# Optimization experiments

Hardware: AMD Instinct MI355X
Metric: run time of the kernel (lower is better)

## Reference

```python
import jax, jax.numpy as jnp
import numpy as np

EPS = 1e-6
NUM_HEADS = 16

def rmsnorm(x, w):
    # x: [..., d], w: [d]
    norm = jax.lax.rsqrt(jnp.mean(x * x, axis=-1, keepdims=True) + EPS)
    return w * (x * norm)

def setup_inputs() -> dict:
    key = jax.random.key(0)
    ks = jax.random.split(key, 6)
    B, N, C = 2, 2048, 1024
    H = NUM_HEADS
    hd = C // H
    x = jax.random.normal(ks[0], (B, N, C), dtype=jnp.float32)
    scale = 1.0 / np.sqrt(C)
    qkv_w = jax.random.normal(ks[1], (C, 3 * C), dtype=jnp.float32) * scale
    qkv_b = jnp.zeros((3 * C,), dtype=jnp.float32)
    q_norm_w = jnp.ones((hd,), dtype=jnp.float32)
    k_norm_w = jnp.ones((hd,), dtype=jnp.float32)
    proj_w = jax.random.normal(ks[2], (C, C), dtype=jnp.float32) * scale
    proj_b = jnp.zeros((C,), dtype=jnp.float32)
    return {"x": x, "qkv_w": qkv_w, "qkv_b": qkv_b,
            "q_norm_w": q_norm_w, "k_norm_w": k_norm_w,
            "proj_w": proj_w, "proj_b": proj_b}

def reference(x, qkv_w, qkv_b, q_norm_w, k_norm_w, proj_w, proj_b):
    B, N, C = x.shape
    H = NUM_HEADS
    hd = C // H
    qkv = x @ qkv_w + qkv_b                       # [B,N,3C]
    qkv = qkv.reshape(B, N, 3, H, hd)
    q, k, v = qkv[:, :, 0], qkv[:, :, 1], qkv[:, :, 2]  # [B,N,H,hd]
    q = jnp.transpose(q, (0, 2, 1, 3))            # [B,H,N,hd]
    k = jnp.transpose(k, (0, 2, 1, 3))
    v = jnp.transpose(v, (0, 2, 1, 3))
    q = rmsnorm(q, q_norm_w)
    k = rmsnorm(k, k_norm_w)
    scores = jnp.einsum('bhqd,bhkd->bhqk', q, k) / jnp.sqrt(jnp.float32(hd))
    attn = jax.nn.softmax(scores, axis=-1)
    out = jnp.einsum('bhqk,bhkd->bhqd', attn, v)  # [B,H,N,hd]
    out = jnp.transpose(out, (0, 2, 1, 3)).reshape(B, N, C)
    return out @ proj_w + proj_b
```

## Files before the change

kernel.cpp:

```cpp
#include <hip/hip_runtime.h>

typedef unsigned short u16;
typedef unsigned int u32;
typedef __bf16 bf16x8 __attribute__((ext_vector_type(8)));
typedef float f32x4 __attribute__((ext_vector_type(4)));
typedef unsigned short u16x8 __attribute__((ext_vector_type(8)));
typedef unsigned short u16x4 __attribute__((ext_vector_type(4)));
typedef float f4 __attribute__((ext_vector_type(4)));

__device__ __forceinline__ float bf2f(u16 u) {
    union { unsigned int i; float f; } c; c.i = ((unsigned int)u) << 16; return c.f;
}
__device__ __forceinline__ u16 f2bf(float f) {
    union { float f; unsigned int i; } c; c.f = f;
    unsigned int r = c.i + 0x7FFFu + ((c.i >> 16) & 1u);
    return (u16)(r >> 16);
}
__device__ __forceinline__ u16 f2bf_rtz(float f) {
    union { float f; unsigned int i; } c; c.f = f;
    return (u16)(c.i >> 16);
}
__device__ __forceinline__ float fast_exp2(float x) {
#if __has_builtin(__builtin_amdgcn_exp2f)
    return __builtin_amdgcn_exp2f(x);
#else
    return exp2f(x);
#endif
}
__device__ __forceinline__ void async16(const void* g, void* l) {
    __builtin_amdgcn_global_load_lds(
        (const __attribute__((address_space(1))) u32*)g,
        (__attribute__((address_space(3))) u32*)l, 16, 0, 0);
}

__global__ __launch_bounds__(256) void cast_bf16(
    const float* __restrict__ X, u16* __restrict__ H)
{
    const size_t i = ((size_t)blockIdx.x * 256 + threadIdx.x) * 8;
    u16x8 h;
    #pragma unroll
    for (int e = 0; e < 8; ++e) h[e] = f2bf(X[i + e]);
    *(u16x8*)&H[i] = h;
}

__global__ __launch_bounds__(256) void transpose_cast(
    const float* __restrict__ W, u16* __restrict__ Th, int K, int N)
{
    __shared__ float tile[32][33];
    const int bk = blockIdx.y * 32, bn = blockIdx.x * 32;
    const int tx = threadIdx.x & 31, ty = threadIdx.x >> 5;
    #pragma unroll
    for (int r = ty; r < 32; r += 8)
        tile[r][tx] = W[(size_t)(bk + r) * N + bn + tx];
    __syncthreads();
    #pragma unroll
    for (int r = ty; r < 32; r += 8)
        Th[(size_t)(bn + r) * K + bk + tx] = f2bf(tile[tx][r]);
}

__global__ __launch_bounds__(256) void gemm_qkv(
    const u16* __restrict__ AH, const u16* __restrict__ BH,
    const float* __restrict__ bias,
    u16* __restrict__ Qb, u16* __restrict__ Kb, u16* __restrict__ Vt,
    const float* __restrict__ qw, const float* __restrict__ kw)
{
    const int K = 1024;
    __shared__ __align__(16) u16 AhT[128 * 32];
    __shared__ __align__(16) u16 BhT[128 * 32];
    const int t = threadIdx.x;
    const int bm = blockIdx.y * 128, bn = blockIdx.x * 128;
    const int wave = t >> 6, lane = t & 63;
    const int wm = (wave >> 1) * 64, wn = (wave & 1) * 64;
    const int l15 = lane & 15, quad = lane >> 4;
    const int srow = lane >> 2, scol = (lane & 3) * 8;

    f32x4 acc[4][4];
    const f32x4 zero = {0.0f, 0.0f, 0.0f, 0.0f};
    #pragma unroll
    for (int i = 0; i < 4; ++i)
        #pragma unroll
        for (int j = 0; j < 4; ++j) acc[i][j] = zero;

    for (int k0 = 0; k0 < K; k0 += 32) {
        #pragma unroll
        for (int rr = 0; rr < 2; ++rr) {
            const int r0 = (rr * 4 + wave) * 16;
            const size_t ga = (size_t)(bm + r0 + srow) * K + k0 + scol;
            const size_t gb = (size_t)(bn + r0 + srow) * K + k0 + scol;
            async16(&AH[ga], &AhT[r0 * 32]);
            async16(&BH[gb], &BhT[r0 * 32]);
        }
        __syncthreads();
        bf16x8 ah[4], bh[4];
        #pragma unroll
        for (int i = 0; i < 4; ++i)
            ah[i] = *(const bf16x8*)&AhT[(wm + i * 16 + l15) * 32 + quad * 8];
        #pragma unroll
        for (int j = 0; j < 4; ++j)
            bh[j] = *(const bf16x8*)&BhT[(wn + j * 16 + l15) * 32 + quad * 8];
        #pragma unroll
        for (int i = 0; i < 4; ++i)
            #pragma unroll
            for (int j = 0; j < 4; ++j)
                acc[i][j] = __builtin_amdgcn_mfma_f32_16x16x32_bf16(
                    ah[i], bh[j], acc[i][j], 0, 0, 0);
        __syncthreads();
    }

    const int gc0 = bn + wn;
    const int sec = gc0 >> 10;
    const int h = (gc0 & 1023) >> 6;
    const int b = bm >> 11;
    const int bhd = b * 16 + h;
    float bv[4], wj[4];
    #pragma unroll
    for (int j = 0; j < 4; ++j) {
        const int d = j * 16 + l15;
        bv[j] = bias[gc0 + d];
        wj[j] = (sec == 2) ? 0.0f : (sec ? kw[d] : qw[d] * 0.18033688011f);
    }
    if (sec < 2) {
        u16* dst = sec ? Kb : Qb;
        #pragma unroll
        for (int i = 0; i < 4; ++i) {
            float val[4][4];
            float ss[4] = {0.0f, 0.0f, 0.0f, 0.0f};
            #pragma unroll
            for (int j = 0; j < 4; ++j)
                #pragma unroll
                for (int r = 0; r < 4; ++r) {
                    val[j][r] = acc[i][j][r] + bv[j];
                    ss[r] += val[j][r] * val[j][r];
                }
            #pragma unroll
            for (int r = 0; r < 4; ++r) {
                #pragma unroll
                for (int m = 1; m < 16; m <<= 1)
                    ss[r] += __shfl_xor(ss[r], m, 64);
                const float nrm = rsqrtf(ss[r] * 0.015625f + 1e-6f);
                const int n = (bm + wm + i * 16 + quad * 4 + r) & 2047;
                const size_t rowb = ((size_t)bhd * 2048 + n) * 64;
                #pragma unroll
                for (int j = 0; j < 4; ++j)
                    dst[rowb + j * 16 + l15] = f2bf(val[j][r] * nrm * wj[j]);
            }
        }
    } else {
        #pragma unroll
        for (int i = 0; i < 4; ++i) {
            const int n0 = (bm + wm + i * 16 + quad * 4) & 2047;
            #pragma unroll
            for (int j = 0; j < 4; ++j) {
                const int d = j * 16 + l15;
                u16x4 pk;
                #pragma unroll
                for (int r = 0; r < 4; ++r)
                    pk[r] = f2bf(acc[i][j][r] + bv[j]);
                *(u16x4*)&Vt[((size_t)bhd * 64 + d) * 2048 + n0] = pk;
            }
        }
    }
}

__global__ __launch_bounds__(256) void gemm_proj(
    const u16* __restrict__ AH, const u16* __restrict__ BH,
    const float* __restrict__ bias, float* __restrict__ C)
{
    const int N = 1024, K = 1024;
    __shared__ __align__(16) u16 AhT[64 * 32];
    __shared__ __align__(16) u16 BhT[128 * 32];
    const int t = threadIdx.x;
    const int bm = blockIdx.y * 64, bn = blockIdx.x * 128;
    const int wave = t >> 6, lane = t & 63;
    const int l15 = lane & 15, quad = lane >> 4;
    const int srow = lane >> 2, scol = (lane & 3) * 8;

    f32x4 acc[4][2];
    const f32x4 zero = {0.0f, 0.0f, 0.0f, 0.0f};
    #pragma unroll
    for (int i = 0; i < 4; ++i)
        #pragma unroll
        for (int j = 0; j < 2; ++j) acc[i][j] = zero;

    for (int k0 = 0; k0 < K; k0 += 32) {
        {
            const int r0 = wave * 16;
            async16(&AH[(size_t)(bm + r0 + srow) * K + k0 + scol],
                    &AhT[r0 * 32]);
        }
        #pragma unroll
        for (int cc = 0; cc < 2; ++cc) {
            const int r0 = (wave * 2 + cc) * 16;
            async16(&BH[(size_t)(bn + r0 + srow) * K + k0 + scol],
                    &BhT[r0 * 32]);
        }
        __syncthreads();
        bf16x8 ah[4], bh[2];
        #pragma unroll
        for (int i = 0; i < 4; ++i)
            ah[i] = *(const bf16x8*)&AhT[(i * 16 + l15) * 32 + quad * 8];
        #pragma unroll
        for (int j = 0; j < 2; ++j)
            bh[j] = *(const bf16x8*)
                &BhT[(wave * 32 + j * 16 + l15) * 32 + quad * 8];
        #pragma unroll
        for (int i = 0; i < 4; ++i)
            #pragma unroll
            for (int j = 0; j < 2; ++j)
                acc[i][j] = __builtin_amdgcn_mfma_f32_16x16x32_bf16(
                    ah[i], bh[j], acc[i][j], 0, 0, 0);
        __syncthreads();
    }

    #pragma unroll
    for (int j = 0; j < 2; ++j) {
        const int col = bn + wave * 32 + j * 16 + l15;
        const float bv = bias[col];
        #pragma unroll
        for (int i = 0; i < 4; ++i) {
            const int row = bm + i * 16 + quad * 4;
            #pragma unroll
            for (int r = 0; r < 4; ++r)
                C[(size_t)(row + r) * N + col] = acc[i][j][r] + bv;
        }
    }
}

__global__ __launch_bounds__(256) void flash_attn_mfma(
    const u16* __restrict__ Qb, const u16* __restrict__ Kb,
    const u16* __restrict__ Vt, u16* __restrict__ Attn)
{
    __shared__ __align__(16) u16 Qlds[128 * 64];
    __shared__ __align__(16) u16 Klds[64 * 64];
    __shared__ __align__(16) u16 Vlds[64 * 64];
    __shared__ __align__(16) u16 Plds[128][72];
    __shared__ float Lbuf[128];

    const int t = threadIdx.x;
    const int qt = blockIdx.x;
    const int bh = blockIdx.y;
    const int n0 = qt * 128;
    const size_t qbase = ((size_t)bh * 2048 + n0) * 64;
    const size_t kbase = (size_t)bh * 2048 * 64;
    const size_t vbase = (size_t)bh * 64 * 2048;
    const int wave = t >> 6, lane = t & 63;
    const int l15 = lane & 15, quad = lane >> 4;
    const int srow8 = lane >> 3;
    const int sgrp = lane & 7;

    #pragma unroll
    for (int c = 0; c < 4; ++c) {
        const int r0 = wave * 32 + c * 8;
        const int row = r0 + srow8;
        const int gg = sgrp ^ (row & 7);
        async16(&Qb[qbase + (size_t)row * 64 + gg * 8], &Qlds[r0 * 64]);
    }
    __syncthreads();

    int kofs[4][2];
    #pragma unroll
    for (int nt = 0; nt < 4; ++nt) {
        const int row = nt * 16 + l15;
        kofs[nt][0] = row * 64 + ((quad ^ (row & 7)) * 8);
        kofs[nt][1] = row * 64 + (((quad + 4) ^ (row & 7)) * 8);
    }
    bf16x8 qf[2][2];
    #pragma unroll
    for (int qs = 0; qs < 2; ++qs) {
        const int row = wave * 32 + qs * 16 + l15;
        qf[qs][0] = *(const bf16x8*)&Qlds[row * 64 + ((quad ^ (row & 7)) * 8)];
        qf[qs][1] = *(const bf16x8*)&Qlds[row * 64 + (((quad + 4) ^ (row & 7)) * 8)];
    }

    f32x4 o[2][4];
    const f32x4 zero = {0.0f, 0.0f, 0.0f, 0.0f};
    #pragma unroll
    for (int qs = 0; qs < 2; ++qs)
        #pragma unroll
        for (int dt = 0; dt < 4; ++dt) o[qs][dt] = zero;
    float lsum[2] = {0.0f, 0.0f};

    for (int kt = 0; kt < 32; ++kt) {
        __syncthreads();
        #pragma unroll
        for (int cc = 0; cc < 2; ++cc) {
            const int r0 = (wave + cc * 4) * 8;
            const int row = r0 + srow8;
            const int gg = sgrp ^ (row & 7);
            async16(&Kb[kbase + (size_t)(kt * 64 + row) * 64 + gg * 8],
                    &Klds[r0 * 64]);
            async16(&Vt[vbase + (size_t)row * 2048 + kt * 64 + gg * 8],
                    &Vlds[r0 * 64]);
        }
        __syncthreads();

        f32x4 s[2][4];
        #pragma unroll
        for (int nt = 0; nt < 4; ++nt) {
            bf16x8 kf0 = *(const bf16x8*)&Klds[kofs[nt][0]];
            bf16x8 kf1 = *(const bf16x8*)&Klds[kofs[nt][1]];
            #pragma unroll
            for (int qs = 0; qs < 2; ++qs) {
                s[qs][nt] = zero;
                s[qs][nt] = __builtin_amdgcn_mfma_f32_16x16x32_bf16(
                    kf0, qf[qs][0], s[qs][nt], 0, 0, 0);
                s[qs][nt] = __builtin_amdgcn_mfma_f32_16x16x32_bf16(
                    kf1, qf[qs][1], s[qs][nt], 0, 0, 0);
            }
        }

        #pragma unroll
        for (int qs = 0; qs < 2; ++qs) {
            const int prow = wave * 32 + qs * 16 + l15;
            #pragma unroll
            for (int nt = 0; nt < 4; ++nt) {
                u16x4 pk;
                #pragma unroll
                for (int r = 0; r < 4; ++r) {
                    const float p = fast_exp2(s[qs][nt][r]);
                    lsum[qs] += p;
                    pk[r] = f2bf_rtz(p);
                }
                *(u16x4*)&Plds[prow][nt * 16 + quad * 4] = pk;
            }
        }

        bf16x8 pf[2][2];
        #pragma unroll
        for (int qs = 0; qs < 2; ++qs) {
            const int prow = wave * 32 + qs * 16 + l15;
            pf[qs][0] = *(const bf16x8*)&Plds[prow][quad * 8];
            pf[qs][1] = *(const bf16x8*)&Plds[prow][quad * 8 + 32];
        }

        #pragma unroll
        for (int dt = 0; dt < 4; ++dt) {
            bf16x8 vf0 = *(const bf16x8*)&Vlds[kofs[dt][0]];
            bf16x8 vf1 = *(const bf16x8*)&Vlds[kofs[dt][1]];
            #pragma unroll
            for (int qs = 0; qs < 2; ++qs) {
                o[qs][dt] = __builtin_amdgcn_mfma_f32_16x16x32_bf16(
                    pf[qs][0], vf0, o[qs][dt], 0, 0, 0);
                o[qs][dt] = __builtin_amdgcn_mfma_f32_16x16x32_bf16(
                    pf[qs][1], vf1, o[qs][dt], 0, 0, 0);
            }
        }
    }

    #pragma unroll
    for (int qs = 0; qs < 2; ++qs) {
        lsum[qs] += __shfl_xor(lsum[qs], 16, 64);
        lsum[qs] += __shfl_xor(lsum[qs], 32, 64);
        if (quad == 0) Lbuf[wave * 32 + qs * 16 + l15] = lsum[qs];
    }
    const size_t obase =
        ((size_t)(bh >> 4) * 2048 + n0) * 1024 + (bh & 15) * 64;
    #pragma unroll
    for (int qs = 0; qs < 2; ++qs)
        #pragma unroll
        for (int r = 0; r < 4; ++r) {
            const float inv =
                1.0f / Lbuf[wave * 32 + qs * 16 + quad * 4 + r];
            const size_t rbase =
                obase + (size_t)(wave * 32 + qs * 16 + quad * 4 + r) * 1024;
            #pragma unroll
            for (int dt = 0; dt < 4; ++dt)
                Attn[rbase + dt * 16 + l15] = f2bf(o[qs][dt][r] * inv);
        }
}

extern "C" void kernel_launch(void* const* d_in, const int* in_sizes, int n_in,
                              void* d_out, int out_size, void* d_ws, size_t ws_size,
                              hipStream_t stream)
{
    const float* x      = (const float*)d_in[0];
    const float* qkv_w  = (const float*)d_in[1];
    const float* qkv_b  = (const float*)d_in[2];
    const float* q_nw   = (const float*)d_in[3];
    const float* k_nw   = (const float*)d_in[4];
    const float* proj_w = (const float*)d_in[5];
    const float* proj_b = (const float*)d_in[6];
    float* out = (float*)d_out;

    char* ws = (char*)d_ws;
    u16* AttnB = (u16*)ws;
    u16* qwT   = (u16*)(ws + 8388608);
    u16* pwT   = (u16*)(ws + 14680064);
    u16* Xb    = (u16*)(ws + 16777216);
    u16* QbB   = (u16*)(ws + 25165824);
    u16* KbB   = (u16*)(ws + 33554432);
    u16* VtB   = (u16*)(ws + 41943040);
    (void)in_sizes; (void)n_in; (void)out_size;
    if (ws_size < 50331648u) return;

    cast_bf16<<<dim3(2048), 256, 0, stream>>>(x, Xb);
    transpose_cast<<<dim3(3072 / 32, 1024 / 32), 256, 0, stream>>>(
        qkv_w, qwT, 1024, 3072);
    transpose_cast<<<dim3(1024 / 32, 1024 / 32), 256, 0, stream>>>(
        proj_w, pwT, 1024, 1024);
    gemm_qkv<<<dim3(3072 / 128, 4096 / 128), 256, 0, stream>>>(
        Xb, qwT, qkv_b, QbB, KbB, VtB, q_nw, k_nw);
    flash_attn_mfma<<<dim3(16, 32), 256, 0, stream>>>(QbB, KbB, VtB, AttnB);
    gemm_proj<<<dim3(1024 / 128, 4096 / 64), 256, 0, stream>>>(
        AttnB, pwT, proj_b, out);
}
```

Baseline: 200.0 us.

## Merge prep kernels and give each attention wave 64 query rows

Folds the activation cast and both weight transpose-casts into one prep launch that dispatches on block index, removing two kernel launches. The flash-attention kernel now runs with 2 waves of 64 query rows each instead of 4 waves of 32, so each K/V fragment read from LDS feeds twice as many MFMAs. Softmax exp is fused directly after each score tile. The cost is higher register pressure per wave and half as many waves per block, which can reduce latency hiding for the K/V loads and barriers.

```diff
diff --git a/kernel.cpp b/kernel.cpp
--- a/kernel.cpp
+++ b/kernel.cpp
@@ -33,22 +33,32 @@
         (__attribute__((address_space(3))) u32*)l, 16, 0, 0);
 }
 
-__global__ __launch_bounds__(256) void cast_bf16(
-    const float* __restrict__ X, u16* __restrict__ H)
-{
-    const size_t i = ((size_t)blockIdx.x * 256 + threadIdx.x) * 8;
-    u16x8 h;
-    #pragma unroll
-    for (int e = 0; e < 8; ++e) h[e] = f2bf(X[i + e]);
-    *(u16x8*)&H[i] = h;
-}
-
-__global__ __launch_bounds__(256) void transpose_cast(
-    const float* __restrict__ W, u16* __restrict__ Th, int K, int N)
+__global__ __launch_bounds__(256) void prep(
+    const float* __restrict__ X, u16* __restrict__ Xb,
+    const float* __restrict__ qkv_w, u16* __restrict__ qwT,
+    const float* __restrict__ proj_w, u16* __restrict__ pwT)
 {
     __shared__ float tile[32][33];
-    const int bk = blockIdx.y * 32, bn = blockIdx.x * 32;
-    const int tx = threadIdx.x & 31, ty = threadIdx.x >> 5;
+    const int blk = blockIdx.x;
+    const int t = threadIdx.x;
+    if (blk < 2048) {
+        const size_t i = ((size_t)blk * 256 + t) * 8;
+        u16x8 h;
+        #pragma unroll
+        for (int e = 0; e < 8; ++e) h[e] = f2bf(X[i + e]);
+        *(u16x8*)&Xb[i] = h;
+        return;
+    }
+    const float* W; u16* Th; int K, N, bx, by;
+    if (blk < 5120) {
+        W = qkv_w; Th = qwT; K = 1024; N = 3072;
+        bx = (blk - 2048) % 96; by = (blk - 2048) / 96;
+    } else {
+        W = proj_w; Th = pwT; K = 1024; N = 1024;
+        bx = (blk - 5120) % 32; by = (blk - 5120) / 32;
+    }
+    const int bk = by * 32, bn = bx * 32;
+    const int tx = t & 31, ty = t >> 5;
     #pragma unroll
     for (int r = ty; r < 32; r += 8)
         tile[r][tx] = W[(size_t)(bk + r) * N + bn + tx];
@@ -226,7 +236,7 @@
     }
 }
 
-__global__ __launch_bounds__(256) void flash_attn_mfma(
+__global__ __launch_bounds__(128) void flash_attn_mfma(
     const u16* __restrict__ Qb, const u16* __restrict__ Kb,
     const u16* __restrict__ Vt, u16* __restrict__ Attn)
 {
@@ -249,8 +259,8 @@
     const int sgrp = lane & 7;
 
     #pragma unroll
-    for (int c = 0; c < 4; ++c) {
-        const int r0 = wave * 32 + c * 8;
+    for (int c = 0; c < 8; ++c) {
+        const int r0 = wave * 64 + c * 8;
         const int row = r0 + srow8;
         const int gg = sgrp ^ (row & 7);
         async16(&Qb[qbase + (size_t)row * 64 + gg * 8], &Qlds[r0 * 64]);
@@ -264,27 +274,27 @@
         kofs[nt][0] = row * 64 + ((quad ^ (row & 7)) * 8);
         kofs[nt][1] = row * 64 + (((quad + 4) ^ (row & 7)) * 8);
     }
-    bf16x8 qf[2][2];
-    #pragma unroll
-    for (int qs = 0; qs < 2; ++qs) {
-        const int row = wave * 32 + qs * 16 + l15;
+    bf16x8 qf[4][2];
+    #pragma unroll
+    for (int qs = 0; qs < 4; ++qs) {
+        const int row = wave * 64 + qs * 16 + l15;
         qf[qs][0] = *(const bf16x8*)&Qlds[row * 64 + ((quad ^ (row & 7)) * 8)];
         qf[qs][1] = *(const bf16x8*)&Qlds[row * 64 + (((quad + 4) ^ (row & 7)) * 8)];
     }
 
-    f32x4 o[2][4];
+    f32x4 o[4][4];
     const f32x4 zero = {0.0f, 0.0f, 0.0f, 0.0f};
     #pragma unroll
-    for (int qs = 0; qs < 2; ++qs)
+    for (int qs = 0; qs < 4; ++qs)
         #pragma unroll
         for (int dt = 0; dt < 4; ++dt) o[qs][dt] = zero;
-    float lsum[2] = {0.0f, 0.0f};
+    float lsum[4] = {0.0f, 0.0f, 0.0f, 0.0f};
 
     for (int kt = 0; kt < 32; ++kt) {
         __syncthreads();
         #pragma unroll
-        for (int cc = 0; cc < 2; ++cc) {
-            const int r0 = (wave + cc * 4) * 8;
+        for (int cc = 0; cc < 4; ++cc) {
+            const int r0 = (wave * 4 + cc) * 8;
             const int row = r0 + srow8;
             const int gg = sgrp ^ (row & 7);
             async16(&Kb[kbase + (size_t)(kt * 64 + row) * 64 + gg * 8],
@@ -294,41 +304,33 @@
         }
         __syncthreads();
 
-        f32x4 s[2][4];
         #pragma unroll
         for (int nt = 0; nt < 4; ++nt) {
             bf16x8 kf0 = *(const bf16x8*)&Klds[kofs[nt][0]];
             bf16x8 kf1 = *(const bf16x8*)&Klds[kofs[nt][1]];
             #pragma unroll
-            for (int qs = 0; qs < 2; ++qs) {
-                s[qs][nt] = zero;
-                s[qs][nt] = __builtin_amdgcn_mfma_f32_16x16x32_bf16(
-                    kf0, qf[qs][0], s[qs][nt], 0, 0, 0);
-                s[qs][nt] = __builtin_amdgcn_mfma_f32_16x16x32_bf16(
-                    kf1, qf[qs][1], s[qs][nt], 0, 0, 0);
-            }
-        }
-
-        #pragma unroll
-        for (int qs = 0; qs < 2; ++qs) {
-            const int prow = wave * 32 + qs * 16 + l15;
-            #pragma unroll
-            for (int nt = 0; nt < 4; ++nt) {
+            for (int qs = 0; qs < 4; ++qs) {
+                f32x4 s = zero;
+                s = __builtin_amdgcn_mfma_f32_16x16x32_bf16(
+                    kf0, qf[qs][0], s, 0, 0, 0);
+                s = __builtin_amdgcn_mfma_f32_16x16x32_bf16(
+                    kf1, qf[qs][1], s, 0, 0, 0);
                 u16x4 pk;
                 #pragma unroll
                 for (int r = 0; r < 4; ++r) {
-                    const float p = fast_exp2(s[qs][nt][r]);
+                    const float p = fast_exp2(s[r]);
                     lsum[qs] += p;
                     pk[r] = f2bf_rtz(p);
                 }
-                *(u16x4*)&Plds[prow][nt * 16 + quad * 4] = pk;
+                *(u16x4*)&Plds[wave * 64 + qs * 16 + l15][nt * 16 + quad * 4]
+                    = pk;
             }
         }
 
-        bf16x8 pf[2][2];
-        #pragma unroll
-        for (int qs = 0; qs < 2; ++qs) {
-            const int prow = wave * 32 + qs * 16 + l15;
+        bf16x8 pf[4][2];
+        #pragma unroll
+        for (int qs = 0; qs < 4; ++qs) {
+            const int prow = wave * 64 + qs * 16 + l15;
             pf[qs][0] = *(const bf16x8*)&Plds[prow][quad * 8];
             pf[qs][1] = *(const bf16x8*)&Plds[prow][quad * 8 + 32];
         }
@@ -338,7 +340,7 @@
             bf16x8 vf0 = *(const bf16x8*)&Vlds[kofs[dt][0]];
             bf16x8 vf1 = *(const bf16x8*)&Vlds[kofs[dt][1]];
             #pragma unroll
-            for (int qs = 0; qs < 2; ++qs) {
+            for (int qs = 0; qs < 4; ++qs) {
                 o[qs][dt] = __builtin_amdgcn_mfma_f32_16x16x32_bf16(
                     pf[qs][0], vf0, o[qs][dt], 0, 0, 0);
                 o[qs][dt] = __builtin_amdgcn_mfma_f32_16x16x32_bf16(
@@ -348,21 +350,21 @@
     }
 
     #pragma unroll
-    for (int qs = 0; qs < 2; ++qs) {
+    for (int qs = 0; qs < 4; ++qs) {
         lsum[qs] += __shfl_xor(lsum[qs], 16, 64);
         lsum[qs] += __shfl_xor(lsum[qs], 32, 64);
-        if (quad == 0) Lbuf[wave * 32 + qs * 16 + l15] = lsum[qs];
+        if (quad == 0) Lbuf[wave * 64 + qs * 16 + l15] = lsum[qs];
     }
     const size_t obase =
         ((size_t)(bh >> 4) * 2048 + n0) * 1024 + (bh & 15) * 64;
     #pragma unroll
-    for (int qs = 0; qs < 2; ++qs)
+    for (int qs = 0; qs < 4; ++qs)
         #pragma unroll
         for (int r = 0; r < 4; ++r) {
             const float inv =
-                1.0f / Lbuf[wave * 32 + qs * 16 + quad * 4 + r];
+                1.0f / Lbuf[wave * 64 + qs * 16 + quad * 4 + r];
             const size_t rbase =
-                obase + (size_t)(wave * 32 + qs * 16 + quad * 4 + r) * 1024;
+                obase + (size_t)(wave * 64 + qs * 16 + quad * 4 + r) * 1024;
             #pragma unroll
             for (int dt = 0; dt < 4; ++dt)
                 Attn[rbase + dt * 16 + l15] = f2bf(o[qs][dt][r] * inv);
@@ -393,14 +395,10 @@
     (void)in_sizes; (void)n_in; (void)out_size;
     if (ws_size < 50331648u) return;
 
-    cast_bf16<<<dim3(2048), 256, 0, stream>>>(x, Xb);
-    transpose_cast<<<dim3(3072 / 32, 1024 / 32), 256, 0, stream>>>(
-        qkv_w, qwT, 1024, 3072);
-    transpose_cast<<<dim3(1024 / 32, 1024 / 32), 256, 0, stream>>>(
-        proj_w, pwT, 1024, 1024);
+    prep<<<dim3(6144), 256, 0, stream>>>(x, Xb, qkv_w, qwT, proj_w, pwT);
     gemm_qkv<<<dim3(3072 / 128, 4096 / 128), 256, 0, stream>>>(
         Xb, qwT, qkv_b, QbB, KbB, VtB, q_nw, k_nw);
-    flash_attn_mfma<<<dim3(16, 32), 256, 0, stream>>>(QbB, KbB, VtB, AttnB);
+    flash_attn_mfma<<<dim3(16, 32), 128, 0, stream>>>(QbB, KbB, VtB, AttnB);
     gemm_proj<<<dim3(1024 / 128, 4096 / 64), 256, 0, stream>>>(
         AttnB, pwT, proj_b, out);
 }
```

Measured after the change: 214.2 us. +7.1%, slower.
